# Kernel tuning notes

Hardware: AMD Instinct MI355X
Metric: run time of the kernel (lower is better)

The kernel has to match this reference:

```python
import jax, jax.numpy as jnp
import numpy as np

EPS_BN = 1e-5
EPS_W = 1e-8


def setup_inputs() -> dict:
    key = jax.random.key(0)
    ks = jax.random.split(key, 6)
    B, N, S, D1, D2 = 8, 8192, 2048, 128, 256
    Cin = D1 + D2  # 384
    return {
        "points_position": jax.random.normal(ks[0], (B, 3, N), jnp.float32),
        "sampled_points_position": jax.random.normal(ks[1], (B, 3, S), jnp.float32),
        "skip_points_feature": jax.random.normal(ks[2], (B, D1, N), jnp.float32),
        "sampled_points_feature": jax.random.normal(ks[3], (B, D2, S), jnp.float32),
        "W1": jax.random.normal(ks[4], (256, Cin), jnp.float32) * 0.05,
        "b1": jnp.zeros((256,), jnp.float32),
        "g1": jnp.ones((256,), jnp.float32),
        "beta1": jnp.zeros((256,), jnp.float32),
        "W2": jax.random.normal(ks[5], (128, 256), jnp.float32) * 0.05,
        "b2": jnp.zeros((128,), jnp.float32),
        "g2": jnp.ones((128,), jnp.float32),
        "beta2": jnp.zeros((128,), jnp.float32),
    }


def _bn_relu(x, g, b):
    # train-mode BatchNorm1d over (batch, points) per channel, x: [B,N,C]
    mean = jnp.mean(x, axis=(0, 1), keepdims=True)
    var = jnp.mean(jnp.square(x - mean), axis=(0, 1), keepdims=True)  # biased var
    return jax.nn.relu((x - mean) * jax.lax.rsqrt(var + EPS_BN) * g + b)


def reference(points_position, sampled_points_position, skip_points_feature,
              sampled_points_feature, W1, b1, g1, beta1, W2, b2, g2, beta2):
    pos = points_position.transpose(0, 2, 1)            # [B,N,3]
    spos = sampled_points_position.transpose(0, 2, 1)   # [B,S,3]
    sfeat = sampled_points_feature.transpose(0, 2, 1)   # [B,S,D2]

    # squared pairwise distance [B,N,S]
    d = (jnp.sum(pos * pos, axis=-1, keepdims=True)
         - 2.0 * jnp.einsum("bnc,bsc->bns", pos, spos)
         + jnp.sum(spos * spos, axis=-1)[:, None, :])

    # 3 nearest neighbors (smallest distances)
    neg_d3, idx = jax.lax.top_k(-d, 3)                  # [B,N,3]
    d3 = -neg_d3
    w = 1.0 / (d3 + EPS_W)
    w = w / jnp.sum(w, axis=-1, keepdims=True)          # [B,N,3]

    gathered = jax.vmap(lambda f, i: f[i])(sfeat, idx)  # [B,N,3,D2]
    interp = jnp.einsum("bnk,bnkd->bnd", w, gathered)   # [B,N,D2]

    feat = jnp.concatenate([skip_points_feature.transpose(0, 2, 1), interp], axis=-1)  # [B,N,D1+D2]

    h = _bn_relu(jnp.einsum("bnc,oc->bno", feat, W1) + b1, g1, beta1)  # [B,N,256]
    h = _bn_relu(jnp.einsum("bnc,oc->bno", h, W2) + b2, g2, beta2)     # [B,N,128]
    return h.transpose(0, 2, 1)                          # [B,128,N]
```

## Files before the change

kernel.cpp:

```cpp
#include <hip/hip_runtime.h>

constexpr int BATCH = 8;
constexpr int NPT   = 8192;
constexpr int NSMP  = 2048;
constexpr int D1C   = 128;
constexpr int D2C   = 256;
constexpr int CIN   = 384;
constexpr int C1    = 256;
constexpr int C2    = 128;
constexpr int BN_TOTAL = BATCH * NPT;

constexpr int GM = 128, GN = 128, GK = 32;

typedef __bf16 bf16x8 __attribute__((ext_vector_type(8)));
typedef short  s16x8  __attribute__((ext_vector_type(8)));
typedef float  f32x4  __attribute__((ext_vector_type(4)));

__device__ __forceinline__ unsigned short f2bf(float x) {
  unsigned u = __builtin_bit_cast(unsigned, x);
  u += 0x7fffu + ((u >> 16) & 1u);
  return (unsigned short)(u >> 16);
}
__device__ __forceinline__ float bf2f(unsigned short h) {
  return __builtin_bit_cast(float, (unsigned)h << 16);
}

__device__ __forceinline__ void gld_lds16(const void* g, void* l) {
  __builtin_amdgcn_global_load_lds(
      (const __attribute__((address_space(1))) void*)g,
      (__attribute__((address_space(3))) void*)l, 16, 0, 0);
}

__global__ void transpose_k(const float* __restrict__ in, float* __restrict__ out,
                            int rows, int cols, long inBatch, long outBatch) {
  __shared__ float tile[32][33];
  const float* inb = in + (size_t)blockIdx.z * inBatch;
  float* outb = out + (size_t)blockIdx.z * outBatch;
  int c0 = blockIdx.x * 32;
  int r0 = blockIdx.y * 32;
  int tx = threadIdx.x, ty = threadIdx.y;
#pragma unroll
  for (int i = 0; i < 32; i += 8) {
    int r = r0 + ty + i;
    tile[ty + i][tx] = inb[(size_t)r * cols + c0 + tx];
  }
  __syncthreads();
#pragma unroll
  for (int i = 0; i < 32; i += 8) {
    int c = c0 + ty + i;
    outb[(size_t)c * rows + r0 + tx] = tile[tx][ty + i];
  }
}

__global__ void skip_to_featB(const float* __restrict__ skip,
                              unsigned short* __restrict__ featB) {
  __shared__ float tile[32][33];
  int b = blockIdx.z;
  int n0 = blockIdx.x * 32;
  int d0 = blockIdx.y * 32;
  int tx = threadIdx.x, ty = threadIdx.y;
#pragma unroll
  for (int i = 0; i < 32; i += 8) {
    tile[ty + i][tx] = skip[((size_t)b * D1C + d0 + ty + i) * NPT + n0 + tx];
  }
  __syncthreads();
#pragma unroll
  for (int i = 0; i < 32; i += 8) {
    int n = n0 + ty + i;
    featB[((size_t)b * NPT + n) * CIN + d0 + tx] = f2bf(tile[tx][ty + i]);
  }
}

__global__ void wprep(const float* __restrict__ W, unsigned short* __restrict__ Wh,
                      int total) {
  int i = blockIdx.x * 256 + threadIdx.x;
  if (i >= total) return;
  Wh[i] = f2bf(W[i]);
}

__global__ void pack_spos(const float* __restrict__ spos, float* __restrict__ sposI) {
  int g = blockIdx.x * 256 + threadIdx.x;
  int b = g >> 11, s = g & (NSMP - 1);
  const float* sp = spos + (size_t)b * 3 * NSMP;
  sposI[(size_t)g * 3 + 0] = sp[s];
  sposI[(size_t)g * 3 + 1] = sp[NSMP + s];
  sposI[(size_t)g * 3 + 2] = sp[2 * NSMP + s];
}

constexpr int SEG = NSMP / 4;

__global__ __launch_bounds__(256) void knn_kernel(
    const float* __restrict__ pos,
    const float* __restrict__ sposI,
    int* __restrict__ idx_out,
    float* __restrict__ wgt_out,
    int* __restrict__ flag_list,
    int* __restrict__ flag_count) {
  __shared__ float qs[3 * NSMP];
  __shared__ float mk[4][4][64];

  int tid = threadIdx.x;
  int wave = tid >> 6, lane = tid & 63;
  int blk = blockIdx.x;
  int b = blk >> 7;
  int n = ((blk & 127) << 6) + lane;

  const float4* src = (const float4*)(sposI + (size_t)b * 3 * NSMP);
  float4* dst = (float4*)qs;
  for (int t = tid; t < 3 * NSMP / 4; t += 256) dst[t] = src[t];
  __syncthreads();

  const float* pb = pos + (size_t)b * 3 * NPT;
  float px = pb[n], py = pb[NPT + n], pz = pb[2 * NPT + n];

  const float INF = __builtin_inff();
  float k0 = INF, k1 = INF, k2 = INF, k3 = INF;

  const float4* q4 = (const float4*)qs;
  int s0 = wave * SEG;

#define KNN_STEP(QX, QY, QZ, SS)                                          \
  {                                                                       \
    float dx = px - (QX), dy = py - (QY), dz = pz - (QZ);                 \
    float d = fmaf(dx, dx, fmaf(dy, dy, dz * dz));                        \
    unsigned ki = (__builtin_bit_cast(unsigned, d) & 0xFFFFF800u) |       \
                  (unsigned)(SS);                                         \
    float kf = __builtin_bit_cast(float, ki);                             \
    float v1 = fmaxf(kf, k0); k0 = fminf(kf, k0);                         \
    float v2 = fmaxf(v1, k1); k1 = fminf(v1, k1);                         \
    float v3 = fmaxf(v2, k2); k2 = fminf(v2, k2);                         \
    k3 = fminf(v3, k3);                                                   \
  }

  for (int t = 0; t < SEG; t += 4) {
    int s = s0 + t;
    int u = 3 * (s >> 2);
    float4 qa = q4[u], qb = q4[u + 1], qc = q4[u + 2];
    KNN_STEP(qa.x, qa.y, qa.z, s + 0)
    KNN_STEP(qa.w, qb.x, qb.y, s + 1)
    KNN_STEP(qb.z, qb.w, qc.x, s + 2)
    KNN_STEP(qc.y, qc.z, qc.w, s + 3)
  }
#undef KNN_STEP

  mk[wave][0][lane] = k0; mk[wave][1][lane] = k1;
  mk[wave][2][lane] = k2; mk[wave][3][lane] = k3;
  __syncthreads();

  if (tid < 64) {
    float K0 = INF, K1 = INF, K2 = INF, K3 = INF;
#pragma unroll
    for (int w = 0; w < 4; w++) {
#pragma unroll
      for (int sl = 0; sl < 4; sl++) {
        float kf = mk[w][sl][tid];
        float v1 = fmaxf(kf, K0); K0 = fminf(kf, K0);
        float v2 = fmaxf(v1, K1); K1 = fminf(v1, K1);
        float v3 = fmaxf(v2, K2); K2 = fminf(v2, K2);
        K3 = fminf(v3, K3);
      }
    }
    int p = blk * 64 + tid;
    int I0 = (int)(__builtin_bit_cast(unsigned, K0) & 0x7FFu);
    int I1 = (int)(__builtin_bit_cast(unsigned, K1) & 0x7FFu);
    int I2 = (int)(__builtin_bit_cast(unsigned, K2) & 0x7FFu);
    float d2m = __builtin_bit_cast(float, __builtin_bit_cast(unsigned, K2) & 0xFFFFF800u);
    float d3m = __builtin_bit_cast(float, __builtin_bit_cast(unsigned, K3) & 0xFFFFF800u);
    bool flag = (d3m - d2m) < 2e-3f * d3m + 1e-7f;
    if (flag) {
      int slot = atomicAdd(flag_count, 1);
      flag_list[slot] = p;
    }
    const float* q = sposI + (size_t)b * 3 * NSMP;
    double pxd = (double)px, pyd = (double)py, pzd = (double)pz;
    double dd[3]; int II[3] = {I0, I1, I2};
#pragma unroll
    for (int k = 0; k < 3; k++) {
      double dx = pxd - (double)q[3 * II[k]];
      double dy = pyd - (double)q[3 * II[k] + 1];
      double dz = pzd - (double)q[3 * II[k] + 2];
      dd[k] = dx * dx + dy * dy + dz * dz;
    }
    double w0 = 1.0 / (dd[0] + 1e-8);
    double w1 = 1.0 / (dd[1] + 1e-8);
    double w2 = 1.0 / (dd[2] + 1e-8);
    double inv = 1.0 / (w0 + w1 + w2);
    size_t o = (size_t)p * 3;
    idx_out[o + 0] = I0; idx_out[o + 1] = I1; idx_out[o + 2] = I2;
    wgt_out[o + 0] = (float)(w0 * inv);
    wgt_out[o + 1] = (float)(w1 * inv);
    wgt_out[o + 2] = (float)(w2 * inv);
  }
}

__device__ __forceinline__ bool dless(double d, int i, double D, int I) {
  return d < D || (d == D && i < I);
}
__device__ __forceinline__ void dins3(double d, int i,
                                      double& b0, double& b1, double& b2,
                                      int& i0, int& i1, int& i2) {
  if (dless(d, i, b2, i2)) {
    if (dless(d, i, b1, i1)) {
      b2 = b1; i2 = i1;
      if (dless(d, i, b0, i0)) { b1 = b0; i1 = i0; b0 = d; i0 = i; }
      else                     { b1 = d; i1 = i; }
    } else { b2 = d; i2 = i; }
  }
}

__global__ __launch_bounds__(256) void knn_fallback(
    const float* __restrict__ pos, const float* __restrict__ sposI,
    const int* __restrict__ flag_list, const int* __restrict__ flag_count,
    int* __restrict__ idx_out, float* __restrict__ wgt_out) {
  int wave = threadIdx.x >> 6, lane = threadIdx.x & 63;
  int gw = blockIdx.x * 4 + wave;
  int cnt = *flag_count;
  for (int t = gw; t < cnt; t += 1024) {
    int p = flag_list[t];
    int b = p >> 13, n = p & (NPT - 1);
    const float* pb = pos + (size_t)b * 3 * NPT;
    double px = (double)pb[n], py = (double)pb[NPT + n], pz = (double)pb[2 * NPT + n];
    const float* q = sposI + (size_t)b * 3 * NSMP;
    double b0 = 1e300, b1 = 1e300, b2 = 1e300;
    int i0 = 0x7FFFFFFF, i1 = 0x7FFFFFFF, i2 = 0x7FFFFFFF;
    for (int s = lane; s < NSMP; s += 64) {
      double dx = px - (double)q[3 * s];
      double dy = py - (double)q[3 * s + 1];
      double dz = pz - (double)q[3 * s + 2];
      double d = dx * dx + dy * dy + dz * dz;
      dins3(d, s, b0, b1, b2, i0, i1, i2);
    }
#pragma unroll
    for (int m = 1; m < 64; m <<= 1) {
      double o0 = __shfl_xor(b0, m, 64), o1 = __shfl_xor(b1, m, 64), o2 = __shfl_xor(b2, m, 64);
      int    j0 = __shfl_xor(i0, m, 64), j1 = __shfl_xor(i1, m, 64), j2 = __shfl_xor(i2, m, 64);
      dins3(o0, j0, b0, b1, b2, i0, i1, i2);
      dins3(o1, j1, b0, b1, b2, i0, i1, i2);
      dins3(o2, j2, b0, b1, b2, i0, i1, i2);
    }
    if (lane == 0) {
      double w0 = 1.0 / (b0 + 1e-8);
      double w1 = 1.0 / (b1 + 1e-8);
      double w2 = 1.0 / (b2 + 1e-8);
      double inv = 1.0 / (w0 + w1 + w2);
      size_t o = (size_t)p * 3;
      idx_out[o + 0] = i0; idx_out[o + 1] = i1; idx_out[o + 2] = i2;
      wgt_out[o + 0] = (float)(w0 * inv);
      wgt_out[o + 1] = (float)(w1 * inv);
      wgt_out[o + 2] = (float)(w2 * inv);
    }
  }
}

__global__ __launch_bounds__(256) void interp_kernel(
    const float* __restrict__ sfeatT,
    const int* __restrict__ idx,
    const float* __restrict__ wgt,
    unsigned short* __restrict__ featB) {
  int p = blockIdx.x;
  int c = threadIdx.x;
  int b = p >> 13;
  size_t o = (size_t)p * 3;
  int i0 = idx[o], i1 = idx[o + 1], i2 = idx[o + 2];
  float w0 = wgt[o], w1 = wgt[o + 1], w2 = wgt[o + 2];
  const float* base = sfeatT + (size_t)b * NSMP * D2C;
  float v = w0 * base[(size_t)i0 * D2C + c]
          + w1 * base[(size_t)i1 * D2C + c]
          + w2 * base[(size_t)i2 * D2C + c];
  featB[(size_t)p * CIN + D1C + c] = f2bf(v);
}

__global__ __launch_bounds__(256) void gemm1_mfma(
    const unsigned short* __restrict__ featB,
    const unsigned short* __restrict__ W1h,
    const float* __restrict__ bias,
    unsigned short* __restrict__ Y1,
    float* __restrict__ sum, float* __restrict__ sumsq) {
  __shared__ __align__(16) unsigned short As[GM * GK];
  __shared__ __align__(16) unsigned short Bs[GN * GK];
  int tid = threadIdx.x;
  int lane = tid & 63;
  int wave = tid >> 6;
  int wrow = (wave >> 1) * 64, wcol = (wave & 1) * 64;
  int m16 = lane & 15, quad = lane >> 4;
  int row0 = blockIdx.x * GM;
  int col0 = blockIdx.y * GN;

  f32x4 acc[4][4];
#pragma unroll
  for (int j = 0; j < 4; j++) {
    float bj = bias[col0 + wcol + j * 16 + m16];
#pragma unroll
    for (int i = 0; i < 4; i++) acc[i][j] = f32x4{bj, bj, bj, bj};
  }

  int rIn  = lane >> 2;
  int col8 = (lane & 3) * 8;

  for (int k0 = 0; k0 < CIN; k0 += GK) {
#pragma unroll
    for (int u = 0; u < 2; u++) {
      int c = wave * 2 + u;
      int row = c * 16 + rIn;
      gld_lds16(&featB[(size_t)(row0 + row) * CIN + k0 + col8], &As[c * 16 * GK]);
      gld_lds16(&W1h [(size_t)(col0 + row) * CIN + k0 + col8], &Bs[c * 16 * GK]);
    }
    __syncthreads();

    bf16x8 a[4], bf[4];
#pragma unroll
    for (int i = 0; i < 4; i++)
      a[i] = __builtin_bit_cast(bf16x8, *(const s16x8*)&As[(wrow + i * 16 + m16) * GK + quad * 8]);
#pragma unroll
    for (int j = 0; j < 4; j++)
      bf[j] = __builtin_bit_cast(bf16x8, *(const s16x8*)&Bs[(wcol + j * 16 + m16) * GK + quad * 8]);
#pragma unroll
    for (int i = 0; i < 4; i++)
#pragma unroll
      for (int j = 0; j < 4; j++)
        acc[i][j] = __builtin_amdgcn_mfma_f32_16x16x32_bf16(a[i], bf[j], acc[i][j], 0, 0, 0);
    __syncthreads();
  }

#pragma unroll
  for (int i = 0; i < 4; i++)
#pragma unroll
    for (int j = 0; j < 4; j++) {
      int col = col0 + wcol + j * 16 + m16;
#pragma unroll
      for (int r = 0; r < 4; r++) {
        int row = row0 + wrow + i * 16 + quad * 4 + r;
        Y1[(size_t)row * C1 + col] = f2bf(acc[i][j][r]);
      }
    }

#pragma unroll
  for (int j = 0; j < 4; j++) {
    float s = 0.f, q = 0.f;
#pragma unroll
    for (int i = 0; i < 4; i++)
#pragma unroll
      for (int r = 0; r < 4; r++) {
        float v = acc[i][j][r];
        s += v; q = fmaf(v, v, q);
      }
    s += __shfl_xor(s, 16, 64); s += __shfl_xor(s, 32, 64);
    q += __shfl_xor(q, 16, 64); q += __shfl_xor(q, 32, 64);
    if (quad == 0) {
      int col = col0 + wcol + j * 16 + m16;
      atomicAdd(&sum[col], s);
      atomicAdd(&sumsq[col], q);
    }
  }
}

__global__ __launch_bounds__(256) void gemm2_mfma(
    const unsigned short* __restrict__ Y1,
    const float* __restrict__ scale1, const float* __restrict__ shift1,
    const unsigned short* __restrict__ W2h,
    const float* __restrict__ bias,
    unsigned short* __restrict__ Y2,
    float* __restrict__ sum, float* __restrict__ sumsq) {
  __shared__ __align__(16) unsigned short As[GM * GK];
  __shared__ __align__(16) unsigned short Bs[GN * GK];
  __shared__ float scs[C1], shs[C1];
  int tid = threadIdx.x;
  int lane = tid & 63;
  int wave = tid >> 6;
  int wrow = (wave >> 1) * 64, wcol = (wave & 1) * 64;
  int m16 = lane & 15, quad = lane >> 4;
  int row0 = blockIdx.x * GM;

  scs[tid] = scale1[tid];
  shs[tid] = shift1[tid];

  f32x4 acc[4][4];
#pragma unroll
  for (int j = 0; j < 4; j++) {
    float bj = bias[wcol + j * 16 + m16];
#pragma unroll
    for (int i = 0; i < 4; i++) acc[i][j] = f32x4{bj, bj, bj, bj};
  }

  int ldr  = tid >> 2;
  int seg  = (tid & 3) * 8;
  int rIn  = lane >> 2;
  int col8 = (lane & 3) * 8;
  __syncthreads();

  for (int k0 = 0; k0 < C1; k0 += GK) {
#pragma unroll
    for (int u = 0; u < 2; u++) {
      int c = wave * 2 + u;
      int row = c * 16 + rIn;
      gld_lds16(&W2h[(size_t)row * C1 + k0 + col8], &Bs[c * 16 * GK]);
    }
#pragma unroll
    for (int rr = 0; rr < 2; rr++) {
      int r = ldr + rr * 64;
      s16x8 v = *(const s16x8*)&Y1[(size_t)(row0 + r) * C1 + k0 + seg];
      unsigned short ov[8];
#pragma unroll
      for (int e = 0; e < 8; e++) {
        float x = bf2f((unsigned short)v[e]);
        float y = fmaxf(fmaf(x, scs[k0 + seg + e], shs[k0 + seg + e]), 0.f);
        ov[e] = f2bf(y);
      }
      *(s16x8*)&As[r * GK + seg] = *(const s16x8*)ov;
    }
    __syncthreads();

    bf16x8 a[4], bf[4];
#pragma unroll
    for (int i = 0; i < 4; i++)
      a[i] = __builtin_bit_cast(bf16x8, *(const s16x8*)&As[(wrow + i * 16 + m16) * GK + quad * 8]);
#pragma unroll
    for (int j = 0; j < 4; j++)
      bf[j] = __builtin_bit_cast(bf16x8, *(const s16x8*)&Bs[(wcol + j * 16 + m16) * GK + quad * 8]);
#pragma unroll
    for (int i = 0; i < 4; i++)
#pragma unroll
      for (int j = 0; j < 4; j++)
        acc[i][j] = __builtin_amdgcn_mfma_f32_16x16x32_bf16(a[i], bf[j], acc[i][j], 0, 0, 0);
    __syncthreads();
  }

#pragma unroll
  for (int i = 0; i < 4; i++)
#pragma unroll
    for (int j = 0; j < 4; j++) {
      int col = wcol + j * 16 + m16;
#pragma unroll
      for (int r = 0; r < 4; r++) {
        int row = row0 + wrow + i * 16 + quad * 4 + r;
        Y2[(size_t)row * C2 + col] = f2bf(acc[i][j][r]);
      }
    }

#pragma unroll
  for (int j = 0; j < 4; j++) {
    float s = 0.f, q = 0.f;
#pragma unroll
    for (int i = 0; i < 4; i++)
#pragma unroll
      for (int r = 0; r < 4; r++) {
        float v = acc[i][j][r];
        s += v; q = fmaf(v, v, q);
      }
    s += __shfl_xor(s, 16, 64); s += __shfl_xor(s, 32, 64);
    q += __shfl_xor(q, 16, 64); q += __shfl_xor(q, 32, 64);
    if (quad == 0) {
      int col = wcol + j * 16 + m16;
      atomicAdd(&sum[col], s);
      atomicAdd(&sumsq[col], q);
    }
  }
}

__global__ void bn_coef_kernel(const float* __restrict__ sum, const float* __restrict__ sumsq,
                               const float* __restrict__ g, const float* __restrict__ beta,
                               float* __restrict__ scale, float* __restrict__ shift, int C) {
  int c = threadIdx.x + blockIdx.x * blockDim.x;
  if (c >= C) return;
  const float invBN = 1.0f / (float)BN_TOTAL;
  float m = sum[c] * invBN;
  float var = sumsq[c] * invBN - m * m;
  float sc = g[c] / sqrtf(var + 1e-5f);
  scale[c] = sc;
  shift[c] = beta[c] - m * sc;
}

__global__ void final_kernel(const unsigned short* __restrict__ Y2,
                             const float* __restrict__ scale, const float* __restrict__ shift,
                             float* __restrict__ out) {
  __shared__ float tile[32][33];
  int b = blockIdx.z;
  int n0 = blockIdx.x * 32;
  int c0 = blockIdx.y * 32;
  int tx = threadIdx.x, ty = threadIdx.y;
  float sc = scale[c0 + tx];
  float sh = shift[c0 + tx];
#pragma unroll
  for (int i = 0; i < 32; i += 8) {
    int n = n0 + ty + i;
    float v = bf2f(Y2[((size_t)b * NPT + n) * C2 + c0 + tx]);
    tile[ty + i][tx] = fmaxf(fmaf(v, sc, sh), 0.f);
  }
  __syncthreads();
#pragma unroll
  for (int i = 0; i < 32; i += 8) {
    int c = c0 + ty + i;
    out[((size_t)b * C2 + c) * NPT + n0 + tx] = tile[tx][ty + i];
  }
}

extern "C" void kernel_launch(void* const* d_in, const int* in_sizes, int n_in,
                              void* d_out, int out_size, void* d_ws, size_t ws_size,
                              hipStream_t stream) {
  (void)in_sizes; (void)n_in; (void)out_size; (void)ws_size;
  const float* pos   = (const float*)d_in[0];
  const float* spos  = (const float*)d_in[1];
  const float* skip  = (const float*)d_in[2];
  const float* sfeat = (const float*)d_in[3];
  const float* W1    = (const float*)d_in[4];
  const float* b1    = (const float*)d_in[5];
  const float* g1    = (const float*)d_in[6];
  const float* beta1 = (const float*)d_in[7];
  const float* W2    = (const float*)d_in[8];
  const float* b2    = (const float*)d_in[9];
  const float* g2    = (const float*)d_in[10];
  const float* beta2 = (const float*)d_in[11];
  float* out = (float*)d_out;

  float* ws = (float*)d_ws;
  size_t off = 0;
  float* sfeatT  = ws + off; off += (size_t)BATCH * NSMP * D2C;
  unsigned short* featB = (unsigned short*)(ws + off); off += (size_t)BN_TOTAL * CIN / 2;
  unsigned short* Y1    = (unsigned short*)(ws + off); off += (size_t)BN_TOTAL * C1 / 2;
  unsigned short* Y2    = (unsigned short*)(ws + off); off += (size_t)BN_TOTAL * C2 / 2;
  unsigned short* W1h   = (unsigned short*)(ws + off); off += (size_t)C1 * CIN / 2;
  unsigned short* W2h   = (unsigned short*)(ws + off); off += (size_t)C2 * C1 / 2;
  int*   knn_idx = (int*)(ws + off); off += (size_t)BN_TOTAL * 3;
  float* knn_w   = ws + off; off += (size_t)BN_TOTAL * 3;
  float* sposI   = ws + off; off += (size_t)BATCH * NSMP * 3;
  int* flag_list = (int*)(ws + off); off += (size_t)BN_TOTAL;
  float* stats   = ws + off; off += 2048;
  float* sum1 = stats, *sumsq1 = stats + 256;
  float* sum2 = stats + 512, *sumsq2 = stats + 640;
  int*   flag_count = (int*)(stats + 768);
  float* scale1 = stats + 1024, *shift1 = stats + 1280;
  float* scale2 = stats + 1536, *shift2 = stats + 1664;

  hipMemsetAsync(stats, 0, 772 * sizeof(float), stream);

  dim3 tb(32, 8);
  transpose_k<<<dim3(NSMP / 32, D2C / 32, BATCH), tb, 0, stream>>>(
      sfeat, sfeatT, D2C, NSMP, (long)D2C * NSMP, (long)NSMP * D2C);
  wprep<<<(C1 * CIN + 255) / 256, 256, 0, stream>>>(W1, W1h, C1 * CIN);
  wprep<<<(C2 * C1 + 255) / 256, 256, 0, stream>>>(W2, W2h, C2 * C1);
  skip_to_featB<<<dim3(NPT / 32, D1C / 32, BATCH), tb, 0, stream>>>(skip, featB);

  pack_spos<<<BATCH * NSMP / 256, 256, 0, stream>>>(spos, sposI);
  knn_kernel<<<BN_TOTAL / 64, 256, 0, stream>>>(pos, sposI, knn_idx, knn_w,
                                                flag_list, flag_count);
  knn_fallback<<<256, 256, 0, stream>>>(pos, sposI, flag_list, flag_count,
                                        knn_idx, knn_w);
  interp_kernel<<<BN_TOTAL, 256, 0, stream>>>(sfeatT, knn_idx, knn_w, featB);

  gemm1_mfma<<<dim3(BN_TOTAL / GM, C1 / GN), 256, 0, stream>>>(
      featB, W1h, b1, Y1, sum1, sumsq1);
  bn_coef_kernel<<<1, C1, 0, stream>>>(sum1, sumsq1, g1, beta1, scale1, shift1, C1);

  gemm2_mfma<<<dim3(BN_TOTAL / GM, 1), 256, 0, stream>>>(
      Y1, scale1, shift1, W2h, b2, Y2, sum2, sumsq2);
  bn_coef_kernel<<<1, C2, 0, stream>>>(sum2, sumsq2, g2, beta2, scale2, shift2, C2);

  final_kernel<<<dim3(NPT / 32, C2 / 32, BATCH), tb, 0, stream>>>(Y2, scale2, shift2, out);
}
```

Before: 345.4 us.

## Use single-wave 128x64 GEMM tiles and replace BN atomics with partial-sum reduction

Both MFMA GEMMs now run with one 64-lane wave per block, each computing a 128x64 output tile (8x4 MFMA fragments) in place of four waves sharing a 128x128 tile. The grid grows, with more, smaller blocks. The per-channel BatchNorm sums are no longer built with global atomics; each row-block writes its partials to a buffer, and a new per-channel reduction kernel sums them and computes scale and shift. The intent is to cut atomic contention and improve occupancy and scheduling. The cost is more accumulator registers per lane, repeated weight loads across blocks, and an extra partial-sum buffer pass.

```diff
diff --git a/kernel.cpp b/kernel.cpp
--- a/kernel.cpp
+++ b/kernel.cpp
@@ -10,7 +10,8 @@
 constexpr int C2    = 128;
 constexpr int BN_TOTAL = BATCH * NPT;
 
-constexpr int GM = 128, GN = 128, GK = 32;
+constexpr int WM = 128, WN = 64, WK = 32;
+constexpr int NRB = BN_TOTAL / WM;
 
 typedef __bf16 bf16x8 __attribute__((ext_vector_type(8)));
 typedef short  s16x8  __attribute__((ext_vector_type(8)));
@@ -270,52 +271,49 @@
   featB[(size_t)p * CIN + D1C + c] = f2bf(v);
 }
 
-__global__ __launch_bounds__(256) void gemm1_mfma(
+__global__ __launch_bounds__(64) void gemm1_wave(
     const unsigned short* __restrict__ featB,
     const unsigned short* __restrict__ W1h,
     const float* __restrict__ bias,
     unsigned short* __restrict__ Y1,
-    float* __restrict__ sum, float* __restrict__ sumsq) {
-  __shared__ __align__(16) unsigned short As[GM * GK];
-  __shared__ __align__(16) unsigned short Bs[GN * GK];
-  int tid = threadIdx.x;
-  int lane = tid & 63;
-  int wave = tid >> 6;
-  int wrow = (wave >> 1) * 64, wcol = (wave & 1) * 64;
+    float* __restrict__ part_s,
+    float* __restrict__ part_q) {
+  __shared__ __align__(16) unsigned short As[WM * WK];
+  __shared__ __align__(16) unsigned short Bs[WN * WK];
+  int lane = threadIdx.x;
   int m16 = lane & 15, quad = lane >> 4;
-  int row0 = blockIdx.x * GM;
-  int col0 = blockIdx.y * GN;
-
-  f32x4 acc[4][4];
+  int rb = blockIdx.x, cb = blockIdx.y;
+  int row0 = rb * WM, col0 = cb * WN;
+  int row16 = lane >> 2, col8 = (lane & 3) * 8;
+
+  f32x4 acc[8][4];
 #pragma unroll
   for (int j = 0; j < 4; j++) {
-    float bj = bias[col0 + wcol + j * 16 + m16];
-#pragma unroll
-    for (int i = 0; i < 4; i++) acc[i][j] = f32x4{bj, bj, bj, bj};
-  }
-
-  int rIn  = lane >> 2;
-  int col8 = (lane & 3) * 8;
-
-  for (int k0 = 0; k0 < CIN; k0 += GK) {
-#pragma unroll
-    for (int u = 0; u < 2; u++) {
-      int c = wave * 2 + u;
-      int row = c * 16 + rIn;
-      gld_lds16(&featB[(size_t)(row0 + row) * CIN + k0 + col8], &As[c * 16 * GK]);
-      gld_lds16(&W1h [(size_t)(col0 + row) * CIN + k0 + col8], &Bs[c * 16 * GK]);
-    }
+    float bj = bias[col0 + j * 16 + m16];
+#pragma unroll
+    for (int i = 0; i < 8; i++) acc[i][j] = f32x4{bj, bj, bj, bj};
+  }
+
+  for (int k0 = 0; k0 < CIN; k0 += WK) {
+#pragma unroll
+    for (int c = 0; c < 8; c++)
+      gld_lds16(&featB[(size_t)(row0 + c * 16 + row16) * CIN + k0 + col8],
+                &As[c * 16 * WK]);
+#pragma unroll
+    for (int c = 0; c < 4; c++)
+      gld_lds16(&W1h[(size_t)(col0 + c * 16 + row16) * CIN + k0 + col8],
+                &Bs[c * 16 * WK]);
     __syncthreads();
 
-    bf16x8 a[4], bf[4];
-#pragma unroll
-    for (int i = 0; i < 4; i++)
-      a[i] = __builtin_bit_cast(bf16x8, *(const s16x8*)&As[(wrow + i * 16 + m16) * GK + quad * 8]);
+    bf16x8 a[8], bf[4];
+#pragma unroll
+    for (int i = 0; i < 8; i++)
+      a[i] = __builtin_bit_cast(bf16x8, *(const s16x8*)&As[(i * 16 + m16) * WK + quad * 8]);
 #pragma unroll
     for (int j = 0; j < 4; j++)
-      bf[j] = __builtin_bit_cast(bf16x8, *(const s16x8*)&Bs[(wcol + j * 16 + m16) * GK + quad * 8]);
-#pragma unroll
-    for (int i = 0; i < 4; i++)
+      bf[j] = __builtin_bit_cast(bf16x8, *(const s16x8*)&Bs[(j * 16 + m16) * WK + quad * 8]);
+#pragma unroll
+    for (int i = 0; i < 8; i++)
 #pragma unroll
       for (int j = 0; j < 4; j++)
         acc[i][j] = __builtin_amdgcn_mfma_f32_16x16x32_bf16(a[i], bf[j], acc[i][j], 0, 0, 0);
@@ -323,102 +321,83 @@
   }
 
 #pragma unroll
-  for (int i = 0; i < 4; i++)
-#pragma unroll
-    for (int j = 0; j < 4; j++) {
-      int col = col0 + wcol + j * 16 + m16;
-#pragma unroll
-      for (int r = 0; r < 4; r++) {
-        int row = row0 + wrow + i * 16 + quad * 4 + r;
-        Y1[(size_t)row * C1 + col] = f2bf(acc[i][j][r]);
-      }
-    }
-
-#pragma unroll
   for (int j = 0; j < 4; j++) {
+    int col = col0 + j * 16 + m16;
     float s = 0.f, q = 0.f;
 #pragma unroll
-    for (int i = 0; i < 4; i++)
+    for (int i = 0; i < 8; i++)
 #pragma unroll
       for (int r = 0; r < 4; r++) {
         float v = acc[i][j][r];
+        Y1[(size_t)(row0 + i * 16 + quad * 4 + r) * C1 + col] = f2bf(v);
         s += v; q = fmaf(v, v, q);
       }
     s += __shfl_xor(s, 16, 64); s += __shfl_xor(s, 32, 64);
     q += __shfl_xor(q, 16, 64); q += __shfl_xor(q, 32, 64);
     if (quad == 0) {
-      int col = col0 + wcol + j * 16 + m16;
-      atomicAdd(&sum[col], s);
-      atomicAdd(&sumsq[col], q);
-    }
-  }
-}
-
-__global__ __launch_bounds__(256) void gemm2_mfma(
+      part_s[(size_t)col * NRB + rb] = s;
+      part_q[(size_t)col * NRB + rb] = q;
+    }
+  }
+}
+
+__global__ __launch_bounds__(64) void gemm2_wave(
     const unsigned short* __restrict__ Y1,
     const float* __restrict__ scale1, const float* __restrict__ shift1,
     const unsigned short* __restrict__ W2h,
     const float* __restrict__ bias,
     unsigned short* __restrict__ Y2,
-    float* __restrict__ sum, float* __restrict__ sumsq) {
-  __shared__ __align__(16) unsigned short As[GM * GK];
-  __shared__ __align__(16) unsigned short Bs[GN * GK];
+    float* __restrict__ part_s,
+    float* __restrict__ part_q) {
+  __shared__ __align__(16) unsigned short As[WM * WK];
+  __shared__ __align__(16) unsigned short Bs[WN * WK];
   __shared__ float scs[C1], shs[C1];
-  int tid = threadIdx.x;
-  int lane = tid & 63;
-  int wave = tid >> 6;
-  int wrow = (wave >> 1) * 64, wcol = (wave & 1) * 64;
+  int lane = threadIdx.x;
   int m16 = lane & 15, quad = lane >> 4;
-  int row0 = blockIdx.x * GM;
-
-  scs[tid] = scale1[tid];
-  shs[tid] = shift1[tid];
-
-  f32x4 acc[4][4];
+  int rb = blockIdx.x, cb = blockIdx.y;
+  int row0 = rb * WM, col0 = cb * WN;
+  int row16 = lane >> 2, col8 = (lane & 3) * 8;
+
+  for (int t = lane; t < C1; t += 64) { scs[t] = scale1[t]; shs[t] = shift1[t]; }
+
+  f32x4 acc[8][4];
 #pragma unroll
   for (int j = 0; j < 4; j++) {
-    float bj = bias[wcol + j * 16 + m16];
-#pragma unroll
-    for (int i = 0; i < 4; i++) acc[i][j] = f32x4{bj, bj, bj, bj};
-  }
-
-  int ldr  = tid >> 2;
-  int seg  = (tid & 3) * 8;
-  int rIn  = lane >> 2;
-  int col8 = (lane & 3) * 8;
-  __syncthreads();
-
-  for (int k0 = 0; k0 < C1; k0 += GK) {
-#pragma unroll
-    for (int u = 0; u < 2; u++) {
-      int c = wave * 2 + u;
-      int row = c * 16 + rIn;
-      gld_lds16(&W2h[(size_t)row * C1 + k0 + col8], &Bs[c * 16 * GK]);
-    }
-#pragma unroll
-    for (int rr = 0; rr < 2; rr++) {
-      int r = ldr + rr * 64;
-      s16x8 v = *(const s16x8*)&Y1[(size_t)(row0 + r) * C1 + k0 + seg];
+    float bj = bias[col0 + j * 16 + m16];
+#pragma unroll
+    for (int i = 0; i < 8; i++) acc[i][j] = f32x4{bj, bj, bj, bj};
+  }
+  __syncthreads();
+
+  for (int k0 = 0; k0 < C1; k0 += WK) {
+#pragma unroll
+    for (int c = 0; c < 4; c++)
+      gld_lds16(&W2h[(size_t)(col0 + c * 16 + row16) * C1 + k0 + col8],
+                &Bs[c * 16 * WK]);
+#pragma unroll
+    for (int c = 0; c < 8; c++) {
+      int row = c * 16 + row16;
+      s16x8 v = *(const s16x8*)&Y1[(size_t)(row0 + row) * C1 + k0 + col8];
       unsigned short ov[8];
 #pragma unroll
       for (int e = 0; e < 8; e++) {
         float x = bf2f((unsigned short)v[e]);
-        float y = fmaxf(fmaf(x, scs[k0 + seg + e], shs[k0 + seg + e]), 0.f);
+        float y = fmaxf(fmaf(x, scs[k0 + col8 + e], shs[k0 + col8 + e]), 0.f);
         ov[e] = f2bf(y);
       }
-      *(s16x8*)&As[r * GK + seg] = *(const s16x8*)ov;
+      *(s16x8*)&As[row * WK + col8] = *(const s16x8*)ov;
     }
     __syncthreads();
 
-    bf16x8 a[4], bf[4];
-#pragma unroll
-    for (int i = 0; i < 4; i++)
-      a[i] = __builtin_bit_cast(bf16x8, *(const s16x8*)&As[(wrow + i * 16 + m16) * GK + quad * 8]);
+    bf16x8 a[8], bf[4];
+#pragma unroll
+    for (int i = 0; i < 8; i++)
+      a[i] = __builtin_bit_cast(bf16x8, *(const s16x8*)&As[(i * 16 + m16) * WK + quad * 8]);
 #pragma unroll
     for (int j = 0; j < 4; j++)
-      bf[j] = __builtin_bit_cast(bf16x8, *(const s16x8*)&Bs[(wcol + j * 16 + m16) * GK + quad * 8]);
-#pragma unroll
-    for (int i = 0; i < 4; i++)
+      bf[j] = __builtin_bit_cast(bf16x8, *(const s16x8*)&Bs[(j * 16 + m16) * WK + quad * 8]);
+#pragma unroll
+    for (int i = 0; i < 8; i++)
 #pragma unroll
       for (int j = 0; j < 4; j++)
         acc[i][j] = __builtin_amdgcn_mfma_f32_16x16x32_bf16(a[i], bf[j], acc[i][j], 0, 0, 0);
@@ -426,48 +405,56 @@
   }
 
 #pragma unroll
-  for (int i = 0; i < 4; i++)
-#pragma unroll
-    for (int j = 0; j < 4; j++) {
-      int col = wcol + j * 16 + m16;
-#pragma unroll
-      for (int r = 0; r < 4; r++) {
-        int row = row0 + wrow + i * 16 + quad * 4 + r;
-        Y2[(size_t)row * C2 + col] = f2bf(acc[i][j][r]);
-      }
-    }
-
-#pragma unroll
   for (int j = 0; j < 4; j++) {
+    int col = col0 + j * 16 + m16;
     float s = 0.f, q = 0.f;
 #pragma unroll
-    for (int i = 0; i < 4; i++)
+    for (int i = 0; i < 8; i++)
 #pragma unroll
       for (int r = 0; r < 4; r++) {
         float v = acc[i][j][r];
+        Y2[(size_t)(row0 + i * 16 + quad * 4 + r) * C2 + col] = f2bf(v);
         s += v; q = fmaf(v, v, q);
       }
     s += __shfl_xor(s, 16, 64); s += __shfl_xor(s, 32, 64);
     q += __shfl_xor(q, 16, 64); q += __shfl_xor(q, 32, 64);
     if (quad == 0) {
-      int col = wcol + j * 16 + m16;
-      atomicAdd(&sum[col], s);
-      atomicAdd(&sumsq[col], q);
-    }
-  }
-}
-
-__global__ void bn_coef_kernel(const float* __restrict__ sum, const float* __restrict__ sumsq,
-                               const float* __restrict__ g, const float* __restrict__ beta,
-                               float* __restrict__ scale, float* __restrict__ shift, int C) {
-  int c = threadIdx.x + blockIdx.x * blockDim.x;
-  if (c >= C) return;
-  const float invBN = 1.0f / (float)BN_TOTAL;
-  float m = sum[c] * invBN;
-  float var = sumsq[c] * invBN - m * m;
-  float sc = g[c] / sqrtf(var + 1e-5f);
-  scale[c] = sc;
-  shift[c] = beta[c] - m * sc;
+      part_s[(size_t)col * NRB + rb] = s;
+      part_q[(size_t)col * NRB + rb] = q;
+    }
+  }
+}
+
+__global__ __launch_bounds__(256) void bn_reduce_coef(
+    const float* __restrict__ part_s, const float* __restrict__ part_q, int nrb,
+    const float* __restrict__ g, const float* __restrict__ beta,
+    float* __restrict__ scale, float* __restrict__ shift) {
+  int ch = blockIdx.x;
+  int tid = threadIdx.x;
+  float s = 0.f, q = 0.f;
+  for (int t = tid; t < nrb; t += 256) {
+    s += part_s[(size_t)ch * nrb + t];
+    q += part_q[(size_t)ch * nrb + t];
+  }
+#pragma unroll
+  for (int m = 1; m < 64; m <<= 1) {
+    s += __shfl_xor(s, m, 64);
+    q += __shfl_xor(q, m, 64);
+  }
+  __shared__ float ls[4], lq[4];
+  int wave = tid >> 6;
+  if ((tid & 63) == 0) { ls[wave] = s; lq[wave] = q; }
+  __syncthreads();
+  if (tid == 0) {
+    s = ls[0] + ls[1] + ls[2] + ls[3];
+    q = lq[0] + lq[1] + lq[2] + lq[3];
+    const float invBN = 1.0f / (float)BN_TOTAL;
+    float mean = s * invBN;
+    float var = q * invBN - mean * mean;
+    float sc = g[ch] / sqrtf(var + 1e-5f);
+    scale[ch] = sc;
+    shift[ch] = beta[ch] - mean * sc;
+  }
 }
 
 __global__ void final_kernel(const unsigned short* __restrict__ Y2,
@@ -524,14 +511,16 @@
   float* knn_w   = ws + off; off += (size_t)BN_TOTAL * 3;
   float* sposI   = ws + off; off += (size_t)BATCH * NSMP * 3;
   int* flag_list = (int*)(ws + off); off += (size_t)BN_TOTAL;
+  float* part1_s = ws + off; off += (size_t)C1 * NRB;
+  float* part1_q = ws + off; off += (size_t)C1 * NRB;
+  float* part2_s = ws + off; off += (size_t)C2 * NRB;
+  float* part2_q = ws + off; off += (size_t)C2 * NRB;
   float* stats   = ws + off; off += 2048;
-  float* sum1 = stats, *sumsq1 = stats + 256;
-  float* sum2 = stats + 512, *sumsq2 = stats + 640;
-  int*   flag_count = (int*)(stats + 768);
-  float* scale1 = stats + 1024, *shift1 = stats + 1280;
-  float* scale2 = stats + 1536, *shift2 = stats + 1664;
-
-  hipMemsetAsync(stats, 0, 772 * sizeof(float), stream);
+  int*   flag_count = (int*)stats;
+  float* scale1 = stats + 256, *shift1 = stats + 512;
+  float* scale2 = stats + 768, *shift2 = stats + 1024;
+
+  hipMemsetAsync(flag_count, 0, sizeof(int), stream);
 
   dim3 tb(32, 8);
   transpose_k<<<dim3(NSMP / 32, D2C / 32, BATCH), tb, 0, stream>>>(
@@ -547,13 +536,13 @@
                                         knn_idx, knn_w);
   interp_kernel<<<BN_TOTAL, 256, 0, stream>>>(sfeatT, knn_idx, knn_w, featB);
 
-  gemm1_mfma<<<dim3(BN_TOTAL / GM, C1 / GN), 256, 0, stream>>>(
-      featB, W1h, b1, Y1, sum1, sumsq1);
-  bn_coef_kernel<<<1, C1, 0, stream>>>(sum1, sumsq1, g1, beta1, scale1, shift1, C1);
-
-  gemm2_mfma<<<dim3(BN_TOTAL / GM, 1), 256, 0, stream>>>(
-      Y1, scale1, shift1, W2h, b2, Y2, sum2, sumsq2);
-  bn_coef_kernel<<<1, C2, 0, stream>>>(sum2, sumsq2, g2, beta2, scale2, shift2, C2);
+  gemm1_wave<<<dim3(NRB, C1 / WN), 64, 0, stream>>>(
+      featB, W1h, b1, Y1, part1_s, part1_q);
+  bn_reduce_coef<<<C1, 256, 0, stream>>>(part1_s, part1_q, NRB, g1, beta1, scale1, shift1);
+
+  gemm2_wave<<<dim3(NRB, C2 / WN), 64, 0, stream>>>(
+      Y1, scale1, shift1, W2h, b2, Y2, part2_s, part2_q);
+  bn_reduce_coef<<<C2, 256, 0, stream>>>(part2_s, part2_q, NRB, g2, beta2, scale2, shift2);
 
   final_kernel<<<dim3(NPT / 32, C2 / 32, BATCH), tb, 0, stream>>>(Y2, scale2, shift2, out);
 }
```

Measured after the change: 315.6 us. 8.6% less time.
